# Performance work log

Measured on AMD Instinct MI355X. Metric: run time of the kernel, lower is better.

## Reference

```python
import jax, jax.numpy as jnp
import numpy as np

N_NODES = 50000
N_EDGES = 1600000
DIM = 128
HEADS = 8
HEAD_DIM = DIM // HEADS


def setup_inputs() -> dict:
    key = jax.random.key(0)
    ks = jax.random.split(key, 12)
    s = 1.0 / np.sqrt(DIM)
    return {
        "x": jax.random.normal(ks[0], (N_NODES, DIM), dtype=jnp.float32),
        "src": jax.random.randint(ks[1], (N_EDGES,), 0, N_NODES, dtype=jnp.int32),
        "dst": jax.random.randint(ks[2], (N_EDGES,), 0, N_NODES, dtype=jnp.int32),
        "Wq": jax.random.uniform(ks[3], (DIM, DIM), jnp.float32, -s, s),
        "bq": jax.random.uniform(ks[4], (DIM,), jnp.float32, -s, s),
        "Wk": jax.random.uniform(ks[5], (DIM, DIM), jnp.float32, -s, s),
        "bk": jax.random.uniform(ks[6], (DIM,), jnp.float32, -s, s),
        "Wv": jax.random.uniform(ks[7], (DIM, DIM), jnp.float32, -s, s),
        "bv": jax.random.uniform(ks[8], (DIM,), jnp.float32, -s, s),
        "Wo": jax.random.uniform(ks[9], (DIM, DIM), jnp.float32, -s, s),
        "bo": jax.random.uniform(ks[10], (DIM,), jnp.float32, -s, s),
    }


def reference(x, src, dst, Wq, bq, Wk, bk, Wv, bv, Wo, bo):
    # Linear projections (torch Linear: x @ W.T + b), split into heads
    q = (x @ Wq.T + bq).reshape(-1, HEADS, HEAD_DIM)  # [N, H, Dh]
    k = (x @ Wk.T + bk).reshape(-1, HEADS, HEAD_DIM)
    v = (x @ Wv.T + bv).reshape(-1, HEADS, HEAD_DIM)

    # u_dot_v: per-edge dot of q[src] and k[dst] per head -> [E, H]
    scores = jnp.einsum("ehd,ehd->eh", q[src], k[dst]) / np.sqrt(HEAD_DIM).astype(np.float32)

    # edge_softmax: softmax over edges grouped by destination node
    m = jax.ops.segment_max(scores, dst, num_segments=N_NODES)  # [N, H]
    e = jnp.exp(scores - m[dst])
    z = jax.ops.segment_sum(e, dst, num_segments=N_NODES)  # [N, H]
    probs = e / z[dst]  # [E, H]

    # u_mul_e_sum: scatter-add of v[src] * probs into dst -> [N, H, Dh]
    msg = v[src] * probs[:, :, None]
    agg = jax.ops.segment_sum(msg, dst, num_segments=N_NODES)

    out = agg.reshape(-1, DIM) @ Wo.T + bo  # dropout p=0.0 -> identity
    return out
```

## Files before the change

### kernel.cpp

```cpp
#include <hip/hip_runtime.h>
#include <hip/hip_bf16.h>
#include <math.h>

#define N_NODES 50000
#define N_EDGES 1600000
#define NBUCK 256
#define NBUCK_ACTIVE ((N_NODES + 255) / 256)
#define P1_BLOCKS ((N_EDGES + 4095) / 4096)
#define CAP 9216
#define QKV_BLOCKS ((N_NODES + 63) / 64)

typedef short bf16x8 __attribute__((ext_vector_type(8)));
typedef float f32x4 __attribute__((ext_vector_type(4)));

#define SC2 0.3606737602222409f
#define MNEG -1.0e30f

static __device__ __forceinline__ unsigned short f2bf(float f) {
  unsigned int b = __float_as_uint(f);
  unsigned int r = (b + 0x7FFFu + ((b >> 16) & 1u)) >> 16;
  return (unsigned short)r;
}
static __device__ __forceinline__ float bf_lo(unsigned int u) {
  return __uint_as_float(u << 16);
}
static __device__ __forceinline__ float bf_hi(unsigned int u) {
  return __uint_as_float(u & 0xFFFF0000u);
}

__global__ __launch_bounds__(256) void bucket_partition(
    const int* __restrict__ src, const int* __restrict__ dst,
    int* __restrict__ bcursor, unsigned int* __restrict__ packed,
    const float* __restrict__ Wq, const float* __restrict__ Wk,
    const float* __restrict__ Wv, const float* __restrict__ Wo,
    unsigned short* __restrict__ wb) {
  const int t = threadIdx.x;
  if (blockIdx.x < 64) {
    int idx = blockIdx.x * 256 + t;
    wb[idx] = f2bf(Wq[idx]);
    wb[16384 + idx] = f2bf(Wk[idx]);
    wb[32768 + idx] = f2bf(Wv[idx]);
    wb[49152 + idx] = f2bf(Wo[idx]);
  }

  __shared__ int h[NBUCK];
  __shared__ int sd[NBUCK];
  __shared__ int lofs[NBUCK];
  __shared__ int gbase[NBUCK];
  __shared__ unsigned int stage[4096];
  __shared__ unsigned short sbin[4096];

  h[t] = 0;
  __syncthreads();
  const int ebase = blockIdx.x * 4096;
  const int count = min(4096, N_EDGES - ebase);
  const int base4 = blockIdx.x * 1024;
  unsigned int val[16];
  int binrank[16];
#pragma unroll
  for (int i = 0; i < 4; ++i) {
    int i4 = base4 + i * 256 + t;
    if (i4 < N_EDGES / 4) {
      int4 s4 = ((const int4*)src)[i4];
      int4 d4 = ((const int4*)dst)[i4];
      int ss[4] = {s4.x, s4.y, s4.z, s4.w};
      int dd[4] = {d4.x, d4.y, d4.z, d4.w};
#pragma unroll
      for (int j = 0; j < 4; ++j) {
        val[i * 4 + j] = ((unsigned)dd[j] << 16) | (unsigned)ss[j];
        int bin = dd[j] >> 8;
        int r = atomicAdd(&h[bin], 1);
        binrank[i * 4 + j] = (bin << 16) | r;
      }
    } else {
#pragma unroll
      for (int j = 0; j < 4; ++j) binrank[i * 4 + j] = -1;
    }
  }
  __syncthreads();
  const int own = h[t];
  if (own > 0) gbase[t] = atomicAdd(&bcursor[t], own);
  sd[t] = own;
  __syncthreads();
  for (int d = 1; d < NBUCK; d <<= 1) {
    int v = (t >= d) ? sd[t - d] : 0;
    __syncthreads();
    sd[t] += v;
    __syncthreads();
  }
  lofs[t] = sd[t] - own;
  __syncthreads();
#pragma unroll
  for (int i = 0; i < 16; ++i) {
    if (binrank[i] >= 0) {
      int bin = binrank[i] >> 16;
      int r = binrank[i] & 0xFFFF;
      int slot = lofs[bin] + r;
      stage[slot] = val[i];
      sbin[slot] = (unsigned short)bin;
    }
  }
  __syncthreads();
  for (int j = t; j < count; j += 256) {
    int b = sbin[j];
    packed[(size_t)b * CAP + gbase[b] + (j - lofs[b])] = stage[j];
  }
}

__global__ __launch_bounds__(256) void qkv_and_finalize(
    const float* __restrict__ x, const unsigned short* __restrict__ wb,
    const float* __restrict__ bq, const float* __restrict__ bk,
    const float* __restrict__ bv,
    unsigned short* __restrict__ qrec, unsigned short* __restrict__ kb,
    unsigned short* __restrict__ vrec,
    const unsigned int* __restrict__ packed, const int* __restrict__ bcursor,
    int* __restrict__ ebeg, int* __restrict__ eend,
    unsigned short* __restrict__ ssrc, int nrows) {
  __shared__ __align__(16) unsigned short sbuf[64 * 136];
  const int tid = threadIdx.x;

  if (blockIdx.x < QKV_BLOCKS) {
    const int w = tid >> 6;
    const int lane = tid & 63;
    const int lr = lane & 15;
    const int kg = lane >> 4;
    const int rowbase = blockIdx.x * 64;
    const int arow = min(rowbase + w * 16 + lr, nrows - 1);

    bf16x8 af[4];
    const float* xr = x + (size_t)arow * 128;
#pragma unroll
    for (int ksub = 0; ksub < 4; ++ksub) {
      const int k0 = ksub * 32 + kg * 8;
      float4 f0 = *(const float4*)(xr + k0);
      float4 f1 = *(const float4*)(xr + k0 + 4);
      af[ksub][0] = (short)f2bf(f0.x);
      af[ksub][1] = (short)f2bf(f0.y);
      af[ksub][2] = (short)f2bf(f0.z);
      af[ksub][3] = (short)f2bf(f0.w);
      af[ksub][4] = (short)f2bf(f1.x);
      af[ksub][5] = (short)f2bf(f1.y);
      af[ksub][6] = (short)f2bf(f1.z);
      af[ksub][7] = (short)f2bf(f1.w);
    }

    for (int p = 0; p < 3; ++p) {
      const unsigned short* wp = wb + p * 16384;
      const float* bias = (p == 0) ? bq : (p == 1) ? bk : bv;
      unsigned short* gout = (p == 0) ? qrec : (p == 1) ? kb : vrec;
      f32x4 acc[8];
#pragma unroll
      for (int nt = 0; nt < 8; ++nt) {
        float b = bias[nt * 16 + lr];
        acc[nt] = (f32x4){b, b, b, b};
      }
#pragma unroll
      for (int ksub = 0; ksub < 4; ++ksub) {
#pragma unroll
        for (int nt = 0; nt < 8; ++nt) {
          bf16x8 bfr = *(const bf16x8*)(wp + (size_t)(nt * 16 + lr) * 128 +
                                        ksub * 32 + kg * 8);
          acc[nt] = __builtin_amdgcn_mfma_f32_16x16x32_bf16(af[ksub], bfr,
                                                            acc[nt], 0, 0, 0);
        }
      }
      __syncthreads();
#pragma unroll
      for (int nt = 0; nt < 8; ++nt) {
        int col = nt * 16 + lr;
#pragma unroll
        for (int r = 0; r < 4; ++r)
          sbuf[(w * 16 + kg * 4 + r) * 136 + col] = f2bf(acc[nt][r]);
      }
      __syncthreads();
#pragma unroll
      for (int i = 0; i < 4; ++i) {
        int idx = i * 256 + tid;
        int lrow = idx >> 4;
        int u16o = (idx & 15) * 8;
        int grow = rowbase + lrow;
        if (grow < nrows)
          *(uint4*)(gout + (size_t)grow * 128 + u16o) =
              *(const uint4*)&sbuf[lrow * 136 + u16o];
      }
    }
  } else {
    int* cnt = (int*)sbuf;
    int* sd = cnt + NBUCK;
    int* cur = sd + NBUCK;
    const int t = tid;
    const int b = blockIdx.x - QKV_BLOCKS;
    const int beg = b * CAP;
    const int n_in_bucket = min(bcursor[b], CAP);
    cnt[t] = 0;
    __syncthreads();
    for (int e = t; e < n_in_bucket; e += 256)
      atomicAdd(&cnt[(packed[beg + e] >> 16) & 255], 1);
    __syncthreads();
    const int own = cnt[t];
    sd[t] = own;
    __syncthreads();
    for (int d = 1; d < NBUCK; d <<= 1) {
      int v = (t >= d) ? sd[t - d] : 0;
      __syncthreads();
      sd[t] += v;
      __syncthreads();
    }
    const int excl = sd[t] - own;
    cur[t] = excl;
    const int node = b * 256 + t;
    if (node < N_NODES) {
      ebeg[node] = beg + excl;
      eend[node] = beg + excl + own;
    }
    __syncthreads();
    for (int e = t; e < n_in_bucket; e += 256) {
      unsigned int p = packed[beg + e];
      int local = (p >> 16) & 255;
      int r = atomicAdd(&cur[local], 1);
      ssrc[beg + r] = (unsigned short)(p & 0xFFFFu);
    }
  }
}

__global__ __launch_bounds__(256) void mfma_out(
    const unsigned short* __restrict__ aggb, const unsigned short* __restrict__ wo,
    const float* __restrict__ bo, float* __restrict__ out, int nrows) {
  const int tid = threadIdx.x;
  const int w = tid >> 6;
  const int lane = tid & 63;
  const int lr = lane & 15;
  const int kg = lane >> 4;
  const int wrow = blockIdx.x * 64 + w * 16;
  const int arow = min(wrow + lr, nrows - 1);

  bf16x8 af[4];
#pragma unroll
  for (int ksub = 0; ksub < 4; ++ksub)
    af[ksub] = *(const bf16x8*)(aggb + (size_t)arow * 128 + ksub * 32 + kg * 8);

  f32x4 acc[8];
#pragma unroll
  for (int nt = 0; nt < 8; ++nt) {
    float b = bo[nt * 16 + lr];
    acc[nt] = (f32x4){b, b, b, b};
  }
#pragma unroll
  for (int ksub = 0; ksub < 4; ++ksub) {
#pragma unroll
    for (int nt = 0; nt < 8; ++nt) {
      bf16x8 bfr = *(const bf16x8*)(wo + (size_t)(nt * 16 + lr) * 128 +
                                    ksub * 32 + kg * 8);
      acc[nt] =
          __builtin_amdgcn_mfma_f32_16x16x32_bf16(af[ksub], bfr, acc[nt], 0, 0, 0);
    }
  }
#pragma unroll
  for (int nt = 0; nt < 8; ++nt) {
    int col = nt * 16 + lr;
#pragma unroll
    for (int r = 0; r < 4; ++r) {
      int grow = wrow + kg * 4 + r;
      if (grow < nrows) out[(size_t)grow * 128 + col] = acc[nt][r];
    }
  }
}

__global__ __launch_bounds__(256, 4) void edge_agg_kernel(
    const unsigned short* __restrict__ qrec, const unsigned short* __restrict__ vrec,
    const unsigned short* __restrict__ kb,
    const int* __restrict__ ebeg, const int* __restrict__ eend,
    const unsigned short* __restrict__ ssrc, unsigned short* __restrict__ aggb) {
  const int wid = threadIdx.x >> 6;
  const int lane = threadIdx.x & 63;
  const int n = blockIdx.x * 4 + wid;
  const int l16 = lane & 15;
  const int qq = lane >> 4;
  const int loff = l16 * 8;

  const uint4 ku = *(const uint4*)(kb + (size_t)n * 128 + loff);
  const float k0 = bf_lo(ku.x), k1 = bf_hi(ku.x), k2 = bf_lo(ku.y), k3 = bf_hi(ku.y);
  const float k4 = bf_lo(ku.z), k5 = bf_hi(ku.z), k6 = bf_lo(ku.w), k7 = bf_hi(ku.w);

  const int start = ebeg[n];
  const int end = eend[n];

  float zz = 0.0f;
  float a0 = 0, a1 = 0, a2 = 0, a3 = 0, a4 = 0, a5 = 0, a6 = 0, a7 = 0;

#define DOT8(t0)                                                       \
  (bf_lo(t0.x) * k0 + bf_hi(t0.x) * k1 + bf_lo(t0.y) * k2 +            \
   bf_hi(t0.y) * k3 + bf_lo(t0.z) * k4 + bf_hi(t0.z) * k5 +            \
   bf_lo(t0.w) * k6 + bf_hi(t0.w) * k7)

#define ACC8(pe, tv)                        \
  a0 = fmaf(pe, bf_lo(tv.x), a0);           \
  a1 = fmaf(pe, bf_hi(tv.x), a1);           \
  a2 = fmaf(pe, bf_lo(tv.y), a2);           \
  a3 = fmaf(pe, bf_hi(tv.y), a3);           \
  a4 = fmaf(pe, bf_lo(tv.z), a4);           \
  a5 = fmaf(pe, bf_hi(tv.z), a5);           \
  a6 = fmaf(pe, bf_lo(tv.w), a6);           \
  a7 = fmaf(pe, bf_hi(tv.w), a7)

  int base = start;
  for (; base + 16 <= end; base += 16) {
    int sA = ssrc[base + qq];
    int sB = ssrc[base + 4 + qq];
    int sC = ssrc[base + 8 + qq];
    int sD = ssrc[base + 12 + qq];
    const uint4 qA = *(const uint4*)(qrec + ((size_t)sA << 7) + loff);
    const uint4 vA = *(const uint4*)(vrec + ((size_t)sA << 7) + loff);
    const uint4 qB = *(const uint4*)(qrec + ((size_t)sB << 7) + loff);
    const uint4 vB = *(const uint4*)(vrec + ((size_t)sB << 7) + loff);
    const uint4 qC = *(const uint4*)(qrec + ((size_t)sC << 7) + loff);
    const uint4 vC = *(const uint4*)(vrec + ((size_t)sC << 7) + loff);
    const uint4 qD = *(const uint4*)(qrec + ((size_t)sD << 7) + loff);
    const uint4 vD = *(const uint4*)(vrec + ((size_t)sD << 7) + loff);

    float pA = DOT8(qA);
    float pB = DOT8(qB);
    float pC = DOT8(qC);
    float pD = DOT8(qD);
    pA += __shfl_xor(pA, 1);
    pB += __shfl_xor(pB, 1);
    pC += __shfl_xor(pC, 1);
    pD += __shfl_xor(pD, 1);
    float peA = __builtin_amdgcn_exp2f(pA * SC2);
    float peB = __builtin_amdgcn_exp2f(pB * SC2);
    float peC = __builtin_amdgcn_exp2f(pC * SC2);
    float peD = __builtin_amdgcn_exp2f(pD * SC2);
    zz += (peA + peB) + (peC + peD);
    ACC8(peA, vA);
    ACC8(peB, vB);
    ACC8(peC, vC);
    ACC8(peD, vD);
  }
  for (; base < end; base += 4) {
    int idx = base + qq;
    bool valid = idx < end;
    int s = ssrc[valid ? idx : end - 1];
    const uint4 q0 = *(const uint4*)(qrec + ((size_t)s << 7) + loff);
    const uint4 v0 = *(const uint4*)(vrec + ((size_t)s << 7) + loff);
    float p = DOT8(q0);
    p += __shfl_xor(p, 1);
    float pe = __builtin_amdgcn_exp2f(valid ? p * SC2 : MNEG);
    zz += pe;
    ACC8(pe, v0);
  }
#undef DOT8
#undef ACC8

#pragma unroll
  for (int off = 16; off <= 32; off <<= 1) {
    zz += __shfl_xor(zz, off);
    a0 += __shfl_xor(a0, off);
    a1 += __shfl_xor(a1, off);
    a2 += __shfl_xor(a2, off);
    a3 += __shfl_xor(a3, off);
    a4 += __shfl_xor(a4, off);
    a5 += __shfl_xor(a5, off);
    a6 += __shfl_xor(a6, off);
    a7 += __shfl_xor(a7, off);
  }
  float inv = (zz > 0.0f) ? 1.0f / zz : 0.0f;

  if (qq == 0) {
    unsigned short o[8] = {f2bf(a0 * inv), f2bf(a1 * inv), f2bf(a2 * inv),
                           f2bf(a3 * inv), f2bf(a4 * inv), f2bf(a5 * inv),
                           f2bf(a6 * inv), f2bf(a7 * inv)};
    *(uint4*)(aggb + (size_t)n * 128 + loff) = *(const uint4*)o;
  }
}

extern "C" void kernel_launch(void* const* d_in, const int* in_sizes, int n_in,
                              void* d_out, int out_size, void* d_ws, size_t ws_size,
                              hipStream_t stream) {
  const float* x  = (const float*)d_in[0];
  const int* src  = (const int*)d_in[1];
  const int* dst  = (const int*)d_in[2];
  const float* Wq = (const float*)d_in[3];
  const float* bq = (const float*)d_in[4];
  const float* Wk = (const float*)d_in[5];
  const float* bk = (const float*)d_in[6];
  const float* Wv = (const float*)d_in[7];
  const float* bv = (const float*)d_in[8];
  const float* Wo = (const float*)d_in[9];
  const float* bo = (const float*)d_in[10];
  float* out = (float*)d_out;

  char* ws = (char*)d_ws;
  size_t off = 0;
  auto carve = [&](size_t bytes) {
    size_t r = off;
    off = (off + bytes + 255) & ~(size_t)255;
    return r;
  };
  unsigned short* qrec = (unsigned short*)(ws + carve((size_t)N_NODES * 256));
  unsigned short* vrec = (unsigned short*)(ws + carve((size_t)N_NODES * 256));
  unsigned short* kb   = (unsigned short*)(ws + carve((size_t)N_NODES * 256));
  unsigned short* aggb = (unsigned short*)(ws + carve((size_t)N_NODES * 256));
  unsigned int* packed = (unsigned int*)(ws + carve((size_t)NBUCK * CAP * 4));
  unsigned short* ssrc = (unsigned short*)(ws + carve((size_t)NBUCK * CAP * 2));
  int* ebeg    = (int*)(ws + carve((size_t)N_NODES * sizeof(int)));
  int* eend    = (int*)(ws + carve((size_t)N_NODES * sizeof(int)));
  int* bcursor = (int*)(ws + carve(NBUCK * sizeof(int)));
  unsigned short* wb = (unsigned short*)(ws + carve((size_t)4 * 128 * 128 * 2));

  hipMemsetAsync(bcursor, 0, NBUCK * sizeof(int), stream);

  bucket_partition<<<P1_BLOCKS, 256, 0, stream>>>(src, dst, bcursor, packed,
                                                  Wq, Wk, Wv, Wo, wb);

  qkv_and_finalize<<<QKV_BLOCKS + NBUCK_ACTIVE, 256, 0, stream>>>(
      x, wb, bq, bk, bv, qrec, kb, vrec, packed, bcursor, ebeg, eend, ssrc,
      N_NODES);

  edge_agg_kernel<<<N_NODES / 4, 256, 0, stream>>>(qrec, vrec, kb, ebeg,
                                                   eend, ssrc, aggb);

  mfma_out<<<QKV_BLOCKS, 256, 0, stream>>>(aggb, wb + 3 * 16384, bo, out,
                                           N_NODES);
}
```

Measured before the change: 196.9 us.

## Fuse edge aggregation with output projection through shared-memory tile

Merges the edge aggregation kernel and the output-projection MFMA kernel into one. Each block now processes 16 nodes (4 per wave, sequentially), stages the bf16 aggregated rows in LDS, then runs the Wo GEMM on that 16-row tile, with each wave computing two 16-column output tiles. This removes the global round-trip of the aggregated buffer and one kernel launch. In exchange each wave handles four nodes serially, there are four times fewer blocks, and a block barrier exposes load imbalance between waves.

Measured after the change: 191.5 us, median of 2. -2.7%, faster.

```diff
diff --git a/kernel.cpp b/kernel.cpp
--- a/kernel.cpp
+++ b/kernel.cpp
@@ -223,70 +223,20 @@
   }
 }
 
-__global__ __launch_bounds__(256) void mfma_out(
-    const unsigned short* __restrict__ aggb, const unsigned short* __restrict__ wo,
-    const float* __restrict__ bo, float* __restrict__ out, int nrows) {
-  const int tid = threadIdx.x;
-  const int w = tid >> 6;
-  const int lane = tid & 63;
-  const int lr = lane & 15;
-  const int kg = lane >> 4;
-  const int wrow = blockIdx.x * 64 + w * 16;
-  const int arow = min(wrow + lr, nrows - 1);
-
-  bf16x8 af[4];
-#pragma unroll
-  for (int ksub = 0; ksub < 4; ++ksub)
-    af[ksub] = *(const bf16x8*)(aggb + (size_t)arow * 128 + ksub * 32 + kg * 8);
-
-  f32x4 acc[8];
-#pragma unroll
-  for (int nt = 0; nt < 8; ++nt) {
-    float b = bo[nt * 16 + lr];
-    acc[nt] = (f32x4){b, b, b, b};
-  }
-#pragma unroll
-  for (int ksub = 0; ksub < 4; ++ksub) {
-#pragma unroll
-    for (int nt = 0; nt < 8; ++nt) {
-      bf16x8 bfr = *(const bf16x8*)(wo + (size_t)(nt * 16 + lr) * 128 +
-                                    ksub * 32 + kg * 8);
-      acc[nt] =
-          __builtin_amdgcn_mfma_f32_16x16x32_bf16(af[ksub], bfr, acc[nt], 0, 0, 0);
-    }
-  }
-#pragma unroll
-  for (int nt = 0; nt < 8; ++nt) {
-    int col = nt * 16 + lr;
-#pragma unroll
-    for (int r = 0; r < 4; ++r) {
-      int grow = wrow + kg * 4 + r;
-      if (grow < nrows) out[(size_t)grow * 128 + col] = acc[nt][r];
-    }
-  }
-}
-
-__global__ __launch_bounds__(256, 4) void edge_agg_kernel(
+__global__ __launch_bounds__(256, 4) void edge_agg_out(
     const unsigned short* __restrict__ qrec, const unsigned short* __restrict__ vrec,
     const unsigned short* __restrict__ kb,
     const int* __restrict__ ebeg, const int* __restrict__ eend,
-    const unsigned short* __restrict__ ssrc, unsigned short* __restrict__ aggb) {
+    const unsigned short* __restrict__ ssrc,
+    const unsigned short* __restrict__ wo, const float* __restrict__ bo,
+    float* __restrict__ out) {
+  __shared__ __align__(16) unsigned short aggs[16 * 136];
   const int wid = threadIdx.x >> 6;
   const int lane = threadIdx.x & 63;
-  const int n = blockIdx.x * 4 + wid;
   const int l16 = lane & 15;
   const int qq = lane >> 4;
   const int loff = l16 * 8;
-
-  const uint4 ku = *(const uint4*)(kb + (size_t)n * 128 + loff);
-  const float k0 = bf_lo(ku.x), k1 = bf_hi(ku.x), k2 = bf_lo(ku.y), k3 = bf_hi(ku.y);
-  const float k4 = bf_lo(ku.z), k5 = bf_hi(ku.z), k6 = bf_lo(ku.w), k7 = bf_hi(ku.w);
-
-  const int start = ebeg[n];
-  const int end = eend[n];
-
-  float zz = 0.0f;
-  float a0 = 0, a1 = 0, a2 = 0, a3 = 0, a4 = 0, a5 = 0, a6 = 0, a7 = 0;
+  const int nbase = blockIdx.x * 16;
 
 #define DOT8(t0)                                                       \
   (bf_lo(t0.x) * k0 + bf_hi(t0.x) * k1 + bf_lo(t0.y) * k2 +            \
@@ -303,73 +253,123 @@
   a6 = fmaf(pe, bf_lo(tv.w), a6);           \
   a7 = fmaf(pe, bf_hi(tv.w), a7)
 
-  int base = start;
-  for (; base + 16 <= end; base += 16) {
-    int sA = ssrc[base + qq];
-    int sB = ssrc[base + 4 + qq];
-    int sC = ssrc[base + 8 + qq];
-    int sD = ssrc[base + 12 + qq];
-    const uint4 qA = *(const uint4*)(qrec + ((size_t)sA << 7) + loff);
-    const uint4 vA = *(const uint4*)(vrec + ((size_t)sA << 7) + loff);
-    const uint4 qB = *(const uint4*)(qrec + ((size_t)sB << 7) + loff);
-    const uint4 vB = *(const uint4*)(vrec + ((size_t)sB << 7) + loff);
-    const uint4 qC = *(const uint4*)(qrec + ((size_t)sC << 7) + loff);
-    const uint4 vC = *(const uint4*)(vrec + ((size_t)sC << 7) + loff);
-    const uint4 qD = *(const uint4*)(qrec + ((size_t)sD << 7) + loff);
-    const uint4 vD = *(const uint4*)(vrec + ((size_t)sD << 7) + loff);
-
-    float pA = DOT8(qA);
-    float pB = DOT8(qB);
-    float pC = DOT8(qC);
-    float pD = DOT8(qD);
-    pA += __shfl_xor(pA, 1);
-    pB += __shfl_xor(pB, 1);
-    pC += __shfl_xor(pC, 1);
-    pD += __shfl_xor(pD, 1);
-    float peA = __builtin_amdgcn_exp2f(pA * SC2);
-    float peB = __builtin_amdgcn_exp2f(pB * SC2);
-    float peC = __builtin_amdgcn_exp2f(pC * SC2);
-    float peD = __builtin_amdgcn_exp2f(pD * SC2);
-    zz += (peA + peB) + (peC + peD);
-    ACC8(peA, vA);
-    ACC8(peB, vB);
-    ACC8(peC, vC);
-    ACC8(peD, vD);
-  }
-  for (; base < end; base += 4) {
-    int idx = base + qq;
-    bool valid = idx < end;
-    int s = ssrc[valid ? idx : end - 1];
-    const uint4 q0 = *(const uint4*)(qrec + ((size_t)s << 7) + loff);
-    const uint4 v0 = *(const uint4*)(vrec + ((size_t)s << 7) + loff);
-    float p = DOT8(q0);
-    p += __shfl_xor(p, 1);
-    float pe = __builtin_amdgcn_exp2f(valid ? p * SC2 : MNEG);
-    zz += pe;
-    ACC8(pe, v0);
+  for (int i = 0; i < 4; ++i) {
+    const int n = nbase + wid * 4 + i;
+    const uint4 ku = *(const uint4*)(kb + (size_t)n * 128 + loff);
+    const float k0 = bf_lo(ku.x), k1 = bf_hi(ku.x);
+    const float k2 = bf_lo(ku.y), k3 = bf_hi(ku.y);
+    const float k4 = bf_lo(ku.z), k5 = bf_hi(ku.z);
+    const float k6 = bf_lo(ku.w), k7 = bf_hi(ku.w);
+
+    const int start = ebeg[n];
+    const int end = eend[n];
+
+    float zz = 0.0f;
+    float a0 = 0, a1 = 0, a2 = 0, a3 = 0, a4 = 0, a5 = 0, a6 = 0, a7 = 0;
+
+    int base = start;
+    for (; base + 16 <= end; base += 16) {
+      int sA = ssrc[base + qq];
+      int sB = ssrc[base + 4 + qq];
+      int sC = ssrc[base + 8 + qq];
+      int sD = ssrc[base + 12 + qq];
+      const uint4 qA = *(const uint4*)(qrec + ((size_t)sA << 7) + loff);
+      const uint4 vA = *(const uint4*)(vrec + ((size_t)sA << 7) + loff);
+      const uint4 qB = *(const uint4*)(qrec + ((size_t)sB << 7) + loff);
+      const uint4 vB = *(const uint4*)(vrec + ((size_t)sB << 7) + loff);
+      const uint4 qC = *(const uint4*)(qrec + ((size_t)sC << 7) + loff);
+      const uint4 vC = *(const uint4*)(vrec + ((size_t)sC << 7) + loff);
+      const uint4 qD = *(const uint4*)(qrec + ((size_t)sD << 7) + loff);
+      const uint4 vD = *(const uint4*)(vrec + ((size_t)sD << 7) + loff);
+
+      float pA = DOT8(qA);
+      float pB = DOT8(qB);
+      float pC = DOT8(qC);
+      float pD = DOT8(qD);
+      pA += __shfl_xor(pA, 1);
+      pB += __shfl_xor(pB, 1);
+      pC += __shfl_xor(pC, 1);
+      pD += __shfl_xor(pD, 1);
+      float peA = __builtin_amdgcn_exp2f(pA * SC2);
+      float peB = __builtin_amdgcn_exp2f(pB * SC2);
+      float peC = __builtin_amdgcn_exp2f(pC * SC2);
+      float peD = __builtin_amdgcn_exp2f(pD * SC2);
+      zz += (peA + peB) + (peC + peD);
+      ACC8(peA, vA);
+      ACC8(peB, vB);
+      ACC8(peC, vC);
+      ACC8(peD, vD);
+    }
+    for (; base < end; base += 4) {
+      int idx = base + qq;
+      bool valid = idx < end;
+      int s = ssrc[valid ? idx : end - 1];
+      const uint4 q0 = *(const uint4*)(qrec + ((size_t)s << 7) + loff);
+      const uint4 v0 = *(const uint4*)(vrec + ((size_t)s << 7) + loff);
+      float p = DOT8(q0);
+      p += __shfl_xor(p, 1);
+      float pe = __builtin_amdgcn_exp2f(valid ? p * SC2 : MNEG);
+      zz += pe;
+      ACC8(pe, v0);
+    }
+
+#pragma unroll
+    for (int off = 16; off <= 32; off <<= 1) {
+      zz += __shfl_xor(zz, off);
+      a0 += __shfl_xor(a0, off);
+      a1 += __shfl_xor(a1, off);
+      a2 += __shfl_xor(a2, off);
+      a3 += __shfl_xor(a3, off);
+      a4 += __shfl_xor(a4, off);
+      a5 += __shfl_xor(a5, off);
+      a6 += __shfl_xor(a6, off);
+      a7 += __shfl_xor(a7, off);
+    }
+    float inv = (zz > 0.0f) ? 1.0f / zz : 0.0f;
+
+    if (qq == 0) {
+      unsigned short o[8] = {f2bf(a0 * inv), f2bf(a1 * inv), f2bf(a2 * inv),
+                             f2bf(a3 * inv), f2bf(a4 * inv), f2bf(a5 * inv),
+                             f2bf(a6 * inv), f2bf(a7 * inv)};
+      *(uint4*)&aggs[(wid * 4 + i) * 136 + loff] = *(const uint4*)o;
+    }
   }
 #undef DOT8
 #undef ACC8
 
-#pragma unroll
-  for (int off = 16; off <= 32; off <<= 1) {
-    zz += __shfl_xor(zz, off);
-    a0 += __shfl_xor(a0, off);
-    a1 += __shfl_xor(a1, off);
-    a2 += __shfl_xor(a2, off);
-    a3 += __shfl_xor(a3, off);
-    a4 += __shfl_xor(a4, off);
-    a5 += __shfl_xor(a5, off);
-    a6 += __shfl_xor(a6, off);
-    a7 += __shfl_xor(a7, off);
-  }
-  float inv = (zz > 0.0f) ? 1.0f / zz : 0.0f;
-
-  if (qq == 0) {
-    unsigned short o[8] = {f2bf(a0 * inv), f2bf(a1 * inv), f2bf(a2 * inv),
-                           f2bf(a3 * inv), f2bf(a4 * inv), f2bf(a5 * inv),
-                           f2bf(a6 * inv), f2bf(a7 * inv)};
-    *(uint4*)(aggb + (size_t)n * 128 + loff) = *(const uint4*)o;
+  __syncthreads();
+
+  bf16x8 af[4];
+#pragma unroll
+  for (int ksub = 0; ksub < 4; ++ksub)
+    af[ksub] = *(const bf16x8*)&aggs[l16 * 136 + ksub * 32 + qq * 8];
+
+  f32x4 acc[2];
+#pragma unroll
+  for (int j = 0; j < 2; ++j) {
+    int nt = wid * 2 + j;
+    float b = bo[nt * 16 + l16];
+    acc[j] = (f32x4){b, b, b, b};
+  }
+#pragma unroll
+  for (int ksub = 0; ksub < 4; ++ksub) {
+#pragma unroll
+    for (int j = 0; j < 2; ++j) {
+      int nt = wid * 2 + j;
+      bf16x8 bfr = *(const bf16x8*)(wo + (size_t)(nt * 16 + l16) * 128 +
+                                    ksub * 32 + qq * 8);
+      acc[j] =
+          __builtin_amdgcn_mfma_f32_16x16x32_bf16(af[ksub], bfr, acc[j], 0, 0, 0);
+    }
+  }
+#pragma unroll
+  for (int j = 0; j < 2; ++j) {
+    int col = (wid * 2 + j) * 16 + l16;
+#pragma unroll
+    for (int r = 0; r < 4; ++r) {
+      int grow = nbase + qq * 4 + r;
+      out[(size_t)grow * 128 + col] = acc[j][r];
+    }
   }
 }
 
@@ -399,7 +399,6 @@
   unsigned short* qrec = (unsigned short*)(ws + carve((size_t)N_NODES * 256));
   unsigned short* vrec = (unsigned short*)(ws + carve((size_t)N_NODES * 256));
   unsigned short* kb   = (unsigned short*)(ws + carve((size_t)N_NODES * 256));
-  unsigned short* aggb = (unsigned short*)(ws + carve((size_t)N_NODES * 256));
   unsigned int* packed = (unsigned int*)(ws + carve((size_t)NBUCK * CAP * 4));
   unsigned short* ssrc = (unsigned short*)(ws + carve((size_t)NBUCK * CAP * 2));
   int* ebeg    = (int*)(ws + carve((size_t)N_NODES * sizeof(int)));
@@ -416,9 +415,6 @@
       x, wb, bq, bk, bv, qrec, kb, vrec, packed, bcursor, ebeg, eend, ssrc,
       N_NODES);
 
-  edge_agg_kernel<<<N_NODES / 4, 256, 0, stream>>>(qrec, vrec, kb, ebeg,
-                                                   eend, ssrc, aggb);
-
-  mfma_out<<<QKV_BLOCKS, 256, 0, stream>>>(aggb, wb + 3 * 16384, bo, out,
-                                           N_NODES);
-}
+  edge_agg_out<<<N_NODES / 16, 256, 0, stream>>>(qrec, vrec, kb, ebeg, eend,
+                                                 ssrc, wb + 3 * 16384, bo, out);
+}
```
